# Optimization experiments

Hardware: AMD Instinct MI355X
Metric: run time of the kernel (lower is better)

## Reference

```python
import jax, jax.numpy as jnp
import numpy as np

EMBED_DIM = 1024
NUM_HEADS = 16
HEAD_WIDTH = 64  # EMBED_DIM == NUM_HEADS * HEAD_WIDTH
B, L = 2, 1024


def setup_inputs() -> dict:
    key = jax.random.key(0)
    ks = jax.random.split(key, 7)
    s = EMBED_DIM ** -0.5
    return {
        "x": jax.random.normal(ks[0], (B, L, EMBED_DIM), dtype=jnp.float32),
        "bias": jax.random.normal(ks[1], (B, L, L, NUM_HEADS), dtype=jnp.float32),
        # nn.Linear weights are (out_features, in_features)
        "w_proj": jax.random.normal(ks[2], (3 * EMBED_DIM, EMBED_DIM), dtype=jnp.float32) * s,
        "w_o": jax.random.normal(ks[3], (EMBED_DIM, EMBED_DIM), dtype=jnp.float32) * s,
        "b_o": jnp.zeros((EMBED_DIM,), dtype=jnp.float32),
        "w_g": jax.random.normal(ks[4], (EMBED_DIM, EMBED_DIM), dtype=jnp.float32) * s,
        "b_g": jnp.ones((EMBED_DIM,), dtype=jnp.float32),
    }


def reference(x, bias, w_proj, w_o, b_o, w_g, b_g):
    b, l, e = x.shape
    h, hw = NUM_HEADS, HEAD_WIDTH
    # fused QKV projection: (B,L,3E) -> (B,H,L,3*hw), head-major split as in torch
    t = jnp.einsum('ble,fe->blf', x, w_proj)
    t = t.reshape(b, l, h, 3 * hw).transpose(0, 2, 1, 3)  # (B,H,L,3hw)
    q, k, v = jnp.split(t, 3, axis=-1)
    q = q * (hw ** -0.5)
    a = jnp.einsum('bhqc,bhkc->bhqk', q, k)
    a = a + bias.transpose(0, 3, 1, 2)  # bias: (B,Lq,Lk,H) -> (B,H,Lq,Lk)
    a = jax.nn.softmax(a, axis=-1)
    y = jnp.einsum('bhqk,bhkc->bqhc', a, v).reshape(b, l, e)
    g = jax.nn.sigmoid(jnp.einsum('ble,fe->blf', x, w_g) + b_g)
    y = g * y
    y = jnp.einsum('ble,fe->blf', y, w_o) + b_o
    # faithful to original rearrange('... lq lk h -> ... h lq lk') applied to (B,h,lq,lk):
    attn = jnp.transpose(a, (0, 3, 1, 2))  # (B, lk, h, lq)
    return y, attn
```

## Files before the change

### kernel.cpp

```cpp
#include <hip/hip_runtime.h>
#include <hip/hip_bf16.h>
#include <stdint.h>

typedef __attribute__((ext_vector_type(4))) float f32x4;
typedef __attribute__((ext_vector_type(8))) short short8;
typedef __attribute__((ext_vector_type(4))) unsigned short u16x4;
typedef unsigned short us;

#define DEV __device__ __forceinline__
#define MFMA16(a, b, c) __builtin_amdgcn_mfma_f32_16x16x32_bf16(a, b, c, 0, 0, 0)

DEV us f2b(float x) {
  union { float f; uint32_t u; } c; c.f = x;
  uint32_t r = (c.u + 0x7fffu + ((c.u >> 16) & 1u)) >> 16;
  return (us)r;
}
DEV float b2f(us x) {
  union { uint32_t u; float f; } c; c.u = ((uint32_t)x) << 16;
  return c.f;
}

DEV void gload_lds16(const void* g, void* l) {
  __builtin_amdgcn_global_load_lds((const __attribute__((address_space(1))) void*)g,
                                   (__attribute__((address_space(3))) void*)l, 16, 0, 0);
}

__global__ __launch_bounds__(256) void prep_k(
    const float* __restrict__ x, const float* __restrict__ wproj,
    const float* __restrict__ wg, const float* __restrict__ wo,
    us* __restrict__ Xbf, us* __restrict__ Wbf, us* __restrict__ Wobf) {
  int i = blockIdx.x * 256 + threadIdx.x;
  const float* src; us* dst;
  if (i < 524288)               { src = x     + (size_t)i * 4;                  dst = Xbf + (size_t)i * 4; }
  else if (i < 524288 + 786432) { int j = i - 524288;            src = wproj + (size_t)j * 4; dst = Wbf + (size_t)j * 4; }
  else if (i < 524288 + 786432 + 262144) { int j = i - (524288 + 786432); src = wg + (size_t)j * 4; dst = Wbf + 3145728 + (size_t)j * 4; }
  else                          { int j = i - (524288 + 786432 + 262144); src = wo + (size_t)j * 4; dst = Wobf + (size_t)j * 4; }
  f32x4 v = *(const f32x4*)src;
  u16x4 o; o.x = f2b(v.x); o.y = f2b(v.y); o.z = f2b(v.z); o.w = f2b(v.w);
  *(u16x4*)dst = o;
}

DEV void gemm_stage(char* sm, const us* A, const us* Bw,
                    int tileMrow, int tileNrow, int buf, int kt, int lane, int wid) {
  const char* gA = (const char*)A;
  const char* gB = (const char*)Bw;
#pragma unroll
  for (int i = 0; i < 2; ++i) {
    int c = wid * 2 + i;
    int off = c * 1024 + lane * 16;
    int r = off >> 6, cb = off & 63;
    gload_lds16(gA + ((size_t)(tileMrow + r) * 2048) + kt * 64 + cb, sm + buf * 8192 + c * 1024);
    gload_lds16(gB + ((size_t)(tileNrow + r) * 2048) + kt * 64 + cb, sm + 16384 + buf * 8192 + c * 1024);
  }
}

DEV void gemm_main(const us* A, const us* Bw,
                   int tileMrow, int tileNrow, f32x4 acc[4][4], char* sm) {
  int tid = threadIdx.x, lane = tid & 63, wid = tid >> 6;
  int wr = wid >> 1, wc = wid & 1;
  gemm_stage(sm, A, Bw, tileMrow, tileNrow, 0, 0, lane, wid);
  for (int kt = 0; kt < 32; ++kt) {
    __syncthreads();
    if (kt < 31) gemm_stage(sm, A, Bw, tileMrow, tileNrow, (kt + 1) & 1, kt + 1, lane, wid);
    int ab = (kt & 1) * 8192;
    int rb = (lane & 15) * 64 + ((lane >> 4) * 16);
    short8 af[4], bf[4];
#pragma unroll
    for (int mi = 0; mi < 4; ++mi)
      af[mi] = *(const short8*)(sm + ab + (wr * 64 + mi * 16) * 64 + rb);
#pragma unroll
    for (int ni = 0; ni < 4; ++ni)
      bf[ni] = *(const short8*)(sm + 16384 + ab + (wc * 64 + ni * 16) * 64 + rb);
#pragma unroll
    for (int mi = 0; mi < 4; ++mi)
#pragma unroll
      for (int ni = 0; ni < 4; ++ni)
        acc[mi][ni] = MFMA16(af[mi], bf[ni], acc[mi][ni]);
  }
}

__global__ __launch_bounds__(256) void gemm_qkvg_k(
    const us* __restrict__ Xbf, const us* __restrict__ Wbf,
    us* __restrict__ Qb, us* __restrict__ Kb, us* __restrict__ Vt,
    float* __restrict__ G, const float* __restrict__ bg) {
  __shared__ char sm[32768];
  int bid = blockIdx.x;
  int swz = (bid & 7) * 64 + (bid >> 3);
  int tileM = swz >> 5, tileN = swz & 31;
  f32x4 acc[4][4] = {};
  gemm_main(Xbf, Wbf, tileM * 128, tileN * 128, acc, sm);
  int lane = threadIdx.x & 63, wid = threadIdx.x >> 6;
  int wr = wid >> 1, wc = wid & 1;
#pragma unroll
  for (int mi = 0; mi < 4; ++mi)
#pragma unroll
    for (int ni = 0; ni < 4; ++ni)
#pragma unroll
      for (int j = 0; j < 4; ++j) {
        int row = tileM * 128 + wr * 64 + mi * 16 + ((lane >> 4) << 2) + j;
        int col = tileN * 128 + wc * 64 + ni * 16 + (lane & 15);
        float v = acc[mi][ni][j];
        int b = row >> 10, l = row & 1023;
        if (col < 3072) {
          int h = col / 192, r = col - h * 192;
          size_t base = ((size_t)(b * 16 + h) * 1024 + l) * 64;
          if (r < 64)        Qb[base + r] = f2b(v * 0.125f);
          else if (r < 128)  Kb[base + (r - 64)] = f2b(v);
          else               Vt[((size_t)(b * 16 + h) * 64 + (r - 128)) * 1024 + l] = f2b(v);
        } else {
          int e = col - 3072;
          float s = v + bg[e];
          G[(size_t)row * 1024 + e] = 1.f / (1.f + __expf(-s));
        }
      }
}

__global__ __launch_bounds__(512) void qke_k(
    const us* __restrict__ Qb, const us* __restrict__ Kb,
    const float* __restrict__ bias, us* __restrict__ E,
    float* __restrict__ lpart) {
  __shared__ float bt[2][16][16][36];
  __shared__ us est[8][2][16][40];
  int tid = threadIdx.x, lane = tid & 63, w = tid >> 6;
  int la = lane & 15, lg = lane >> 4;
  int bid = blockIdx.x;
  int b = (bid & 7) >> 2, kc = bid & 3;
  int qt = bid >> 3;
  int lq0 = qt * 16, lk00 = kc * 256;

  short8 qf[2][2];
#pragma unroll
  for (int s = 0; s < 2; ++s) {
    size_t bh = (size_t)(b * 16 + w * 2 + s);
#pragma unroll
    for (int ks = 0; ks < 2; ++ks)
      qf[s][ks] = *(const short8*)(Qb + bh * 65536 + (size_t)(lq0 + la) * 64 + ks * 32 + lg * 8);
  }
  const float* bsrc = bias + ((size_t)b << 24) + ((size_t)lq0 << 14);

  f32x4 vv[4];
#pragma unroll
  for (int i = 0; i < 4; ++i) {
    int f = i * 512 + tid;
    int h4 = f & 3, lk = (f >> 2) & 31, q = f >> 7;
    vv[i] = *(const f32x4*)(bsrc + ((size_t)q << 14) + ((size_t)(lk00 + lk) << 4) + h4 * 4);
  }
#pragma unroll
  for (int i = 0; i < 4; ++i) {
    int f = i * 512 + tid;
    int h4 = f & 3, lk = (f >> 2) & 31, q = f >> 7;
#pragma unroll
    for (int e = 0; e < 4; ++e) {
      int h = h4 * 4 + e;
      bt[0][h][q][lk ^ ((h & 7) << 2)] = vv[i][e];
    }
  }

  float lacc[2] = {0.f, 0.f};
#pragma unroll 1
  for (int t = 0; t < 8; ++t) {
    __syncthreads();
    if (t < 7) {
      int lkt = lk00 + (t + 1) * 32;
#pragma unroll
      for (int i = 0; i < 4; ++i) {
        int f = i * 512 + tid;
        int h4 = f & 3, lk = (f >> 2) & 31, q = f >> 7;
        vv[i] = *(const f32x4*)(bsrc + ((size_t)q << 14) + ((size_t)(lkt + lk) << 4) + h4 * 4);
      }
    }
    int cb = t & 1;
    int lkg = lk00 + t * 32;
#pragma unroll
    for (int s = 0; s < 2; ++s) {
      int h = w * 2 + s;
      const us* Kh = Kb + (size_t)(b * 16 + h) * 65536;
#pragma unroll
      for (int fr = 0; fr < 2; ++fr) {
        const us* kr = Kh + (size_t)(lkg + fr * 16 + la) * 64 + lg * 8;
        short8 kf0 = *(const short8*)kr;
        short8 kf1 = *(const short8*)(kr + 32);
        int lkb = (fr * 16 + lg * 4) ^ ((h & 7) << 2);
        f32x4 a = *(const f32x4*)&bt[cb][h][la][lkb];
        a = MFMA16(kf0, qf[s][0], a);
        a = MFMA16(kf1, qf[s][1], a);
        u16x4 ev;
#pragma unroll
        for (int j = 0; j < 4; ++j) {
          float e = __expf(a[j]);
          lacc[s] += e;
          ev[j] = f2b(e);
        }
        *(u16x4*)&est[w][s][la][fr * 16 + lg * 4] = ev;
      }
      {
        int q = lane >> 2, bo = (lane & 3) * 8;
        short8 ev8 = *(const short8*)&est[w][s][q][bo];
        *(short8*)(E + (((size_t)(b * 1024 + lq0 + q) * 16 + h) << 10) + lkg + bo) = ev8;
      }
    }
    if (t < 7) {
      int nb = (t + 1) & 1;
#pragma unroll
      for (int i = 0; i < 4; ++i) {
        int f = i * 512 + tid;
        int h4 = f & 3, lk = (f >> 2) & 31, q = f >> 7;
#pragma unroll
        for (int e = 0; e < 4; ++e) {
          int h = h4 * 4 + e;
          bt[nb][h][q][lk ^ ((h & 7) << 2)] = vv[i][e];
        }
      }
    }
  }
#pragma unroll
  for (int s = 0; s < 2; ++s) {
    float v = lacc[s];
    v += __shfl_xor(v, 16);
    v += __shfl_xor(v, 32);
    if (lg == 0) lpart[kc * 32768 + (b * 16 + w * 2 + s) * 1024 + lq0 + la] = v;
  }
}

__global__ __launch_bounds__(256) void pv_k(
    const us* __restrict__ E, const us* __restrict__ Vt,
    const float* __restrict__ lpart, const float* __restrict__ G,
    float* __restrict__ outa, us* __restrict__ Ybf) {
  __shared__ char sm[49792];
  float* lv = (float*)(sm + 49664);
  int tid = threadIdx.x, lane = tid & 63, w = tid >> 6;
  int la = lane & 15, lg = lane >> 4;
  int bid = blockIdx.x;
  int g = bid >> 8, qt = (bid >> 3) & 31, xx = bid & 7;
  int bh = g * 8 + xx;
  int b = bh >> 4, h = bh & 15;
  int qb = qt * 32;
  if (tid < 32) {
    int r = bh * 1024 + qb + tid;
    float s = lpart[r] + lpart[32768 + r] + lpart[65536 + r] + lpart[98304 + r];
    lv[tid] = 1.f / s;
  }
  __syncthreads();
  char* pb = sm + w * 4096;
  const us* Vh = Vt + (size_t)bh * 65536;
  f32x4 yacc[2][4] = {};
  int lkw = w * 256;

#pragma unroll 1
  for (int cc = 0; cc < 4; ++cc) {
    int lk0 = lkw + cc * 64;
#pragma unroll
    for (int it = 0; it < 4; ++it) {
      int ci = it * 64 + lane;
      int q = ci >> 3, c16 = ci & 7;
      short8 ev = *(const short8*)(E + (((size_t)(b * 1024 + qb + q) * 16 + h) << 10) + lk0 + c16 * 8);
      *(short8*)(pb + q * 128 + ((c16 * 16) ^ ((q & 7) << 4))) = ev;
    }
#pragma unroll
    for (int it = 0; it < 8; ++it) {
      int idx = it * 64 + lane;
      int lkL = idx >> 3, q4 = idx & 7;
      f32x4 ov;
#pragma unroll
      for (int i = 0; i < 4; ++i) {
        int q = q4 * 4 + i;
        us e = *(const us*)(pb + q * 128 + ((2 * lkL) ^ ((q & 7) << 4)));
        ov[i] = b2f(e) * lv[q];
      }
      *(f32x4*)(outa + (((size_t)(b * 1024 + lk0 + lkL) * 16 + h) << 10) + qb + q4 * 4) = ov;
    }
#pragma unroll
    for (int ks = 0; ks < 2; ++ks) {
      short8 pa[2];
#pragma unroll
      for (int qh = 0; qh < 2; ++qh) {
        int row = qh * 16 + la;
        pa[qh] = *(const short8*)(pb + row * 128 + ((ks * 64 + lg * 16) ^ ((row & 7) << 4)));
      }
#pragma unroll
      for (int ni = 0; ni < 4; ++ni) {
        short8 vf = *(const short8*)(Vh + (size_t)(ni * 16 + la) * 1024 + lk0 + ks * 32 + lg * 8);
        yacc[0][ni] = MFMA16(pa[0], vf, yacc[0][ni]);
        yacc[1][ni] = MFMA16(pa[1], vf, yacc[1][ni]);
      }
    }
  }

  float* red = (float*)(sm + 16384);
#pragma unroll
  for (int qh = 0; qh < 2; ++qh)
#pragma unroll
    for (int ni = 0; ni < 4; ++ni)
#pragma unroll
      for (int j = 0; j < 4; ++j) {
        int r = qh * 16 + lg * 4 + j, c = ni * 16 + la;
        red[w * 2080 + r * 65 + c] = yacc[qh][ni][j];
      }
  __syncthreads();
#pragma unroll
  for (int rr = 0; rr < 8; ++rr) {
    int e = rr * 256 + tid;
    int r = e >> 6, c = e & 63;
    float s = red[r * 65 + c] + red[2080 + r * 65 + c] +
              red[4160 + r * 65 + c] + red[6240 + r * 65 + c];
    size_t gi = (((size_t)(b * 1024 + qb + r)) << 10) + h * 64 + c;
    Ybf[gi] = f2b(s * lv[r] * G[gi]);
  }
}

__global__ __launch_bounds__(256) void gemm_out_k(
    const us* __restrict__ Ybf, const us* __restrict__ Wobf,
    const float* __restrict__ bo, float* __restrict__ outy) {
  __shared__ char sm[32768];
  int bid = blockIdx.x;
  int swz = (bid & 7) * 16 + (bid >> 3);
  int tileM = swz >> 3, tileN = swz & 7;
  f32x4 acc[4][4] = {};
  gemm_main(Ybf, Wobf, tileM * 128, tileN * 128, acc, sm);
  int lane = threadIdx.x & 63, wid = threadIdx.x >> 6;
  int wr = wid >> 1, wc = wid & 1;
#pragma unroll
  for (int mi = 0; mi < 4; ++mi)
#pragma unroll
    for (int ni = 0; ni < 4; ++ni)
#pragma unroll
      for (int j = 0; j < 4; ++j) {
        int row = tileM * 128 + wr * 64 + mi * 16 + ((lane >> 4) << 2) + j;
        int col = tileN * 128 + wc * 64 + ni * 16 + (lane & 15);
        outy[(size_t)row * 1024 + col] = acc[mi][ni][j] + bo[col];
      }
}

extern "C" void kernel_launch(void* const* d_in, const int* in_sizes, int n_in,
                              void* d_out, int out_size, void* d_ws, size_t ws_size,
                              hipStream_t stream) {
  const float* x     = (const float*)d_in[0];
  const float* bias  = (const float*)d_in[1];
  const float* wproj = (const float*)d_in[2];
  const float* wo    = (const float*)d_in[3];
  const float* bo    = (const float*)d_in[4];
  const float* wg    = (const float*)d_in[5];
  const float* bg    = (const float*)d_in[6];
  float* outy = (float*)d_out;
  float* outa = outy + 2097152;

  char* ws = (char*)d_ws;
  us*    Xbf  = (us*)(ws);
  us*    Wbf  = (us*)(ws + 4  * 1024 * 1024);
  us*    Wobf = (us*)(ws + 12 * 1024 * 1024);
  us*    Qb   = (us*)(ws + 14 * 1024 * 1024);
  us*    Kb   = (us*)(ws + 18 * 1024 * 1024);
  us*    Vt   = (us*)(ws + 22 * 1024 * 1024);
  float* G    = (float*)(ws + 26 * 1024 * 1024);
  us*    Ybf  = (us*)(ws + 34 * 1024 * 1024);
  float* lpart= (float*)(ws + (size_t)38 * 1024 * 1024);
  us*    E    = (us*)   (ws + (size_t)40 * 1024 * 1024);
  if (ws_size < (size_t)104 * 1024 * 1024) return;

  prep_k<<<dim3(7168), dim3(256), 0, stream>>>(x, wproj, wg, wo, Xbf, Wbf, Wobf);
  gemm_qkvg_k<<<dim3(512), dim3(256), 0, stream>>>(Xbf, Wbf, Qb, Kb, Vt, G, bg);
  qke_k<<<dim3(512), dim3(512), 0, stream>>>(Qb, Kb, bias, E, lpart);
  pv_k<<<dim3(1024), dim3(256), 0, stream>>>(E, Vt, lpart, G, outa, Ybf);
  gemm_out_k<<<dim3(128), dim3(256), 0, stream>>>(Ybf, Wobf, bo, outy);
}
```

Measured before the change: 206.0 us.

## Load bias tiles directly into LDS and write exp scores straight to global

The bias tile prefetch now uses direct global-to-LDS loads in the native (q, lk, h) layout instead of loading into registers and scattering transposed into a swizzled LDS buffer. Each lane gathers its four bias values from LDS with scalar reads. The LDS staging buffer for the exp scores is removed, so each lane writes 8-byte chunks to E directly. This cuts register pressure and VALU/LDS scatter work and frees LDS, but the strided scalar LDS reads may bank-conflict and the 8-byte global stores are less coalesced than the earlier 16-byte row writes.

Result: no change. 202.2 us (-1.9%).

```diff
diff --git a/kernel.cpp b/kernel.cpp
--- a/kernel.cpp
+++ b/kernel.cpp
@@ -119,8 +119,7 @@
     const us* __restrict__ Qb, const us* __restrict__ Kb,
     const float* __restrict__ bias, us* __restrict__ E,
     float* __restrict__ lpart) {
-  __shared__ float bt[2][16][16][36];
-  __shared__ us est[8][2][16][40];
+  __shared__ float bt[2][16][516];
   int tid = threadIdx.x, lane = tid & 63, w = tid >> 6;
   int la = lane & 15, lg = lane >> 4;
   int bid = blockIdx.x;
@@ -136,24 +135,13 @@
     for (int ks = 0; ks < 2; ++ks)
       qf[s][ks] = *(const short8*)(Qb + bh * 65536 + (size_t)(lq0 + la) * 64 + ks * 32 + lg * 8);
   }
-  const float* bsrc = bias + ((size_t)b << 24) + ((size_t)lq0 << 14);
-
-  f32x4 vv[4];
+  const char* bsrc = (const char*)(bias + ((size_t)b << 24) + ((size_t)lq0 << 14));
+
 #pragma unroll
   for (int i = 0; i < 4; ++i) {
-    int f = i * 512 + tid;
-    int h4 = f & 3, lk = (f >> 2) & 31, q = f >> 7;
-    vv[i] = *(const f32x4*)(bsrc + ((size_t)q << 14) + ((size_t)(lk00 + lk) << 4) + h4 * 4);
-  }
-#pragma unroll
-  for (int i = 0; i < 4; ++i) {
-    int f = i * 512 + tid;
-    int h4 = f & 3, lk = (f >> 2) & 31, q = f >> 7;
-#pragma unroll
-    for (int e = 0; e < 4; ++e) {
-      int h = h4 * 4 + e;
-      bt[0][h][q][lk ^ ((h & 7) << 2)] = vv[i][e];
-    }
+    int q = w * 2 + (i >> 1), half = i & 1;
+    gload_lds16(bsrc + ((size_t)q << 16) + ((size_t)(lk00 + half * 16) << 6) + lane * 16,
+                (char*)&bt[0][q][half * 256] + lane * 16);
   }
 
   float lacc[2] = {0.f, 0.f};
@@ -162,11 +150,12 @@
     __syncthreads();
     if (t < 7) {
       int lkt = lk00 + (t + 1) * 32;
+      int nb = (t + 1) & 1;
 #pragma unroll
       for (int i = 0; i < 4; ++i) {
-        int f = i * 512 + tid;
-        int h4 = f & 3, lk = (f >> 2) & 31, q = f >> 7;
-        vv[i] = *(const f32x4*)(bsrc + ((size_t)q << 14) + ((size_t)(lkt + lk) << 4) + h4 * 4);
+        int q = w * 2 + (i >> 1), half = i & 1;
+        gload_lds16(bsrc + ((size_t)q << 16) + ((size_t)(lkt + half * 16) << 6) + lane * 16,
+                    (char*)&bt[nb][q][half * 256] + lane * 16);
       }
     }
     int cb = t & 1;
@@ -180,8 +169,10 @@
         const us* kr = Kh + (size_t)(lkg + fr * 16 + la) * 64 + lg * 8;
         short8 kf0 = *(const short8*)kr;
         short8 kf1 = *(const short8*)(kr + 32);
-        int lkb = (fr * 16 + lg * 4) ^ ((h & 7) << 2);
-        f32x4 a = *(const f32x4*)&bt[cb][h][la][lkb];
+        f32x4 a;
+#pragma unroll
+        for (int j = 0; j < 4; ++j)
+          a[j] = bt[cb][la][(fr * 16 + lg * 4 + j) * 16 + h];
         a = MFMA16(kf0, qf[s][0], a);
         a = MFMA16(kf1, qf[s][1], a);
         u16x4 ev;
@@ -191,25 +182,7 @@
           lacc[s] += e;
           ev[j] = f2b(e);
         }
-        *(u16x4*)&est[w][s][la][fr * 16 + lg * 4] = ev;
-      }
-      {
-        int q = lane >> 2, bo = (lane & 3) * 8;
-        short8 ev8 = *(const short8*)&est[w][s][q][bo];
-        *(short8*)(E + (((size_t)(b * 1024 + lq0 + q) * 16 + h) << 10) + lkg + bo) = ev8;
-      }
-    }
-    if (t < 7) {
-      int nb = (t + 1) & 1;
-#pragma unroll
-      for (int i = 0; i < 4; ++i) {
-        int f = i * 512 + tid;
-        int h4 = f & 3, lk = (f >> 2) & 31, q = f >> 7;
-#pragma unroll
-        for (int e = 0; e < 4; ++e) {
-          int h = h4 * 4 + e;
-          bt[nb][h][q][lk ^ ((h & 7) << 2)] = vv[i][e];
-        }
+        *(u16x4*)(E + (((size_t)(b * 1024 + lq0 + la) * 16 + h) << 10) + lkg + fr * 16 + lg * 4) = ev;
       }
     }
   }
```
